# Kernel tuning notes

Measured on AMD Instinct MI355X. Metric: run time of the kernel, lower is better.

## Reference

```python
import jax, jax.numpy as jnp
import numpy as np

LAMBD = 1.0  # margin, matches init kwarg lambd
N, C, D = 16384, 4096, 128


def setup_inputs() -> dict:
    key = jax.random.key(0)
    k1, k2, k3 = jax.random.split(key, 3)
    embeddings = jax.random.normal(k1, (N, D), dtype=jnp.float32)
    targets = jax.random.randint(k2, (N,), 0, C, dtype=jnp.int64)
    centers = jax.random.normal(k3, (C, D), dtype=jnp.float32)
    return {"embeddings": embeddings, "targets": targets, "centers": centers}


def reference(embeddings, targets, centers):
    # Squared euclidean distances from every sample to every center, [n, C],
    # via ||e||^2 + ||c||^2 - 2 e.c (avoids the [n, C, d] broadcast tensor).
    e2 = jnp.sum(embeddings * embeddings, axis=-1, keepdims=True)          # [n, 1]
    c2 = jnp.sum(centers * centers, axis=-1)                               # [C]
    dist = e2 + c2[None, :] - 2.0 * jnp.matmul(embeddings, centers.T)      # [n, C]

    tgt = targets.astype(jnp.int32)
    ap = jnp.take_along_axis(dist, tgt[:, None], axis=1)                   # [n, 1]

    # loss_val[i, c] = lambd + d(e_i, center_{y_i}) - d(e_i, center_c)
    loss_val = LAMBD + ap - dist                                           # [n, C]

    # Triplet (i, y_i, c) is mined iff loss_val > 0 and c != y_i.
    not_label = jnp.arange(dist.shape[1], dtype=jnp.int32)[None, :] != tgt[:, None]
    mask = (loss_val > 0.0) & not_label

    # For mined triplets relu(ap - an + lambd) == loss_val (already > 0).
    total = jnp.sum(jnp.where(mask, loss_val, 0.0))
    cnt = jnp.sum(mask).astype(loss_val.dtype)
    # If no triplet violates the margin, the original returns 0.
    return jnp.where(cnt > 0.0, total / jnp.maximum(cnt, 1.0), 0.0)
```

## Files before the change

kernel.cpp:

```cpp
#include <hip/hip_runtime.h>

#define N_SAMP 16384
#define N_CENT 4096
#define DIM    128
#define LAMBD  1.0f
#define NSLOT  256

typedef _Float16 half8  __attribute__((ext_vector_type(8)));
typedef float    floatx4 __attribute__((ext_vector_type(4)));

struct Slot { float sum; unsigned int cnt; unsigned int pad[30]; };

__device__ __forceinline__ void gload_lds16(const void* g, void* l) {
  __builtin_amdgcn_global_load_lds(
      (__attribute__((address_space(1))) void*)(g),
      (__attribute__((address_space(3))) void*)(l), 16, 0, 0);
}

__global__ __launch_bounds__(256) void prep_kernel(
    const float* __restrict__ E, const float* __restrict__ Cc,
    const int* __restrict__ tgt,
    _Float16* __restrict__ Eh, _Float16* __restrict__ Ch,
    float* __restrict__ c2, float* __restrict__ rowk,
    Slot* __restrict__ slots) {
  const int tid = threadIdx.x;
  const int STAT_BLOCKS = (N_SAMP + N_CENT) / 16;
  if ((int)blockIdx.x < STAT_BLOCKS) {
    if (blockIdx.x == 0) { slots[tid].sum = 0.f; slots[tid].cnt = 0u; }
    const int row   = blockIdx.x * 16 + (tid >> 4);
    const int l16   = tid & 15;
    if (row < N_SAMP) {
      const int yi = tgt[row];
      const float4* e = (const float4*)(E  + (size_t)row * DIM + l16 * 8);
      const float4* c = (const float4*)(Cc + (size_t)yi  * DIM + l16 * 8);
      float4 e0 = e[0], e1 = e[1], c0 = c[0], c1 = c[1];
      float s = c0.x*(c0.x-2.f*e0.x) + c0.y*(c0.y-2.f*e0.y)
              + c0.z*(c0.z-2.f*e0.z) + c0.w*(c0.w-2.f*e0.w)
              + c1.x*(c1.x-2.f*e1.x) + c1.y*(c1.y-2.f*e1.y)
              + c1.z*(c1.z-2.f*e1.z) + c1.w*(c1.w-2.f*e1.w);
      s += __shfl_down(s, 8, 16);
      s += __shfl_down(s, 4, 16);
      s += __shfl_down(s, 2, 16);
      s += __shfl_down(s, 1, 16);
      if (l16 == 0) rowk[row] = LAMBD + s;
    } else {
      const int cI = row - N_SAMP;
      const float4* c = (const float4*)(Cc + (size_t)cI * DIM + l16 * 8);
      float4 c0 = c[0], c1 = c[1];
      float s = c0.x*c0.x + c0.y*c0.y + c0.z*c0.z + c0.w*c0.w
              + c1.x*c1.x + c1.y*c1.y + c1.z*c1.z + c1.w*c1.w;
      s += __shfl_down(s, 8, 16);
      s += __shfl_down(s, 4, 16);
      s += __shfl_down(s, 2, 16);
      s += __shfl_down(s, 1, 16);
      if (l16 == 0) c2[cI] = s;
    }
  } else {
    const int t = ((int)blockIdx.x - STAT_BLOCKS) * 256 + tid;
    const int NE8 = N_SAMP * DIM / 8;
    const float4* src;
    half8* dst;
    int idx;
    if (t < NE8) { src = (const float4*)E;  dst = (half8*)Eh; idx = t; }
    else         { src = (const float4*)Cc; dst = (half8*)Ch; idx = t - NE8; }
    float4 a = src[(size_t)idx * 2], b = src[(size_t)idx * 2 + 1];
    half8 h;
    h[0]=(_Float16)a.x; h[1]=(_Float16)a.y; h[2]=(_Float16)a.z; h[3]=(_Float16)a.w;
    h[4]=(_Float16)b.x; h[5]=(_Float16)b.y; h[6]=(_Float16)b.z; h[7]=(_Float16)b.w;
    dst[idx] = h;
  }
}

__global__ __launch_bounds__(256, 3) void center_gemm_kernel(
    const _Float16* __restrict__ Eh, const _Float16* __restrict__ Ch,
    const float* __restrict__ c2, const float* __restrict__ rowk,
    const int* __restrict__ tgt,
    Slot* __restrict__ slots) {
  __shared__ _Float16 Bs[128 * DIM];
  __shared__ float rowkS[128];
  __shared__ float c2S[128];
  __shared__ int   yS[128];
  __shared__ float swsum[4];
  __shared__ int   swcnt[4];

  const int tid  = threadIdx.x;
  const int w    = tid >> 6;
  const int lane = tid & 63;
  const int q = lane >> 4, r = lane & 15;

  const int bid = blockIdx.x;
  const int xcd = bid & 7;
  const int j   = bid >> 3;
  const int bm  = xcd * 16 + (j & 15);
  const int bn  = j >> 4;

  {
    const char* gB = (const char*)(Ch + (size_t)bn * 128 * DIM);
    char* lB = (char*)Bs;
    const int p  = lane & 15;
    const int r4 = lane >> 4;
    #pragma unroll
    for (int it = 0; it < 8; ++it) {
      const int off = (w * 8 + it) * 1024;
      const int row = (w * 8 + it) * 4 + r4;
      const int gof = row * 256 + (p ^ (row & 15)) * 16;
      gload_lds16(gB + gof, lB + off);
    }
  }

  const int wm = w >> 1, wn = w & 1;
  const int row0 = wm * 64, col0 = wn * 64;
  half8 areg[4][4];
  #pragma unroll
  for (int ks = 0; ks < 4; ++ks)
    #pragma unroll
    for (int mt = 0; mt < 4; ++mt)
      areg[ks][mt] = *(const half8*)&Eh[
          (size_t)(bm * 128 + row0 + mt * 16 + r) * DIM + ks * 32 + q * 8];

  if (tid < 128) {
    rowkS[tid] = rowk[bm * 128 + tid];
    yS[tid]    = tgt[bm * 128 + tid];
    c2S[tid]   = c2[bn * 128 + tid];
  }
  __syncthreads();

  floatx4 acc[4][4];
  #pragma unroll
  for (int a = 0; a < 4; ++a)
    #pragma unroll
    for (int b = 0; b < 4; ++b)
      acc[a][b] = (floatx4){0.f, 0.f, 0.f, 0.f};

  #pragma unroll
  for (int ks = 0; ks < 4; ++ks) {
    const int cidx = ks * 4 + q;
    half8 bf[4];
    #pragma unroll
    for (int nt = 0; nt < 4; ++nt)
      bf[nt] = *(const half8*)&Bs[(col0 + nt * 16 + r) * DIM + ((cidx ^ r) * 8)];
    #pragma unroll
    for (int mt = 0; mt < 4; ++mt)
      #pragma unroll
      for (int nt = 0; nt < 4; ++nt)
        acc[mt][nt] = __builtin_amdgcn_mfma_f32_16x16x32_f16(areg[ks][mt], bf[nt], acc[mt][nt], 0, 0, 0);
  }

  float lsum = 0.f;
  int   lcnt = 0;
  #pragma unroll
  for (int mt = 0; mt < 4; ++mt) {
    float rk[4]; int yv[4];
    #pragma unroll
    for (int rg = 0; rg < 4; ++rg) {
      const int row = row0 + mt * 16 + q * 4 + rg;
      rk[rg] = rowkS[row];
      yv[rg] = yS[row];
    }
    #pragma unroll
    for (int nt = 0; nt < 4; ++nt) {
      const int col  = col0 + nt * 16 + r;
      const float c2v = c2S[col];
      const int gcol = bn * 128 + col;
      #pragma unroll
      for (int rg = 0; rg < 4; ++rg) {
        const float v = rk[rg] + 2.f * acc[mt][nt][rg] - c2v;
        const bool mined = (v > 0.f) & (gcol != yv[rg]);
        lsum += mined ? v : 0.f;
        lcnt += mined ? 1 : 0;
      }
    }
  }

  #pragma unroll
  for (int off = 32; off > 0; off >>= 1) {
    lsum += __shfl_down(lsum, off);
    lcnt += __shfl_down(lcnt, off);
  }
  if (lane == 0) { swsum[w] = lsum; swcnt[w] = lcnt; }
  __syncthreads();
  if (tid == 0) {
    const float s = swsum[0] + swsum[1] + swsum[2] + swsum[3];
    const int   c = swcnt[0] + swcnt[1] + swcnt[2] + swcnt[3];
    Slot* sl = &slots[bid & (NSLOT - 1)];
    atomicAdd(&sl->sum, s);
    atomicAdd(&sl->cnt, (unsigned int)c);
  }
}

__global__ __launch_bounds__(256) void finalize_kernel(
    const Slot* __restrict__ slots, float* __restrict__ out) {
  const int tid = threadIdx.x;
  float s = slots[tid].sum;
  unsigned int c = slots[tid].cnt;
  #pragma unroll
  for (int off = 32; off > 0; off >>= 1) {
    s += __shfl_down(s, off);
    c += __shfl_down(c, off);
  }
  __shared__ float ss[4];
  __shared__ unsigned int sc[4];
  if ((tid & 63) == 0) { ss[tid >> 6] = s; sc[tid >> 6] = c; }
  __syncthreads();
  if (tid == 0) {
    const float S = ss[0] + ss[1] + ss[2] + ss[3];
    const unsigned int C = sc[0] + sc[1] + sc[2] + sc[3];
    out[0] = (C > 0u) ? (S / (float)C) : 0.f;
  }
}

__global__ void zero_kernel(float* ws_sum, unsigned int* ws_cnt) {
  if (threadIdx.x == 0) { *ws_sum = 0.f; *ws_cnt = 0u; }
}

__global__ void finalize_simple(const float* __restrict__ ws_sum,
                                const unsigned int* __restrict__ ws_cnt,
                                float* __restrict__ out) {
  if (threadIdx.x == 0 && blockIdx.x == 0) {
    const unsigned int c = *ws_cnt;
    out[0] = (c > 0u) ? (*ws_sum / (float)c) : 0.f;
  }
}

__global__ __launch_bounds__(256) void fallback_kernel(
    const float* __restrict__ E, const float* __restrict__ Cc,
    const int* __restrict__ tgt,
    float* __restrict__ ws_sum, unsigned int* __restrict__ ws_cnt) {
  __shared__ float eS[DIM];
  __shared__ float apS;
  const int i = blockIdx.x;
  const int tid = threadIdx.x;
  if (tid < DIM) eS[tid] = E[(size_t)i * DIM + tid];
  __syncthreads();
  const int yi = tgt[i];
  float dloc[16];
  #pragma unroll
  for (int j = 0; j < 16; ++j) {
    const int c = tid + 256 * j;
    const float* cp = Cc + (size_t)c * DIM;
    float s = 0.f;
    for (int d = 0; d < DIM; d += 4) {
      float4 cv = *(const float4*)(cp + d);
      s += cv.x * (cv.x - 2.f * eS[d + 0]) + cv.y * (cv.y - 2.f * eS[d + 1])
         + cv.z * (cv.z - 2.f * eS[d + 2]) + cv.w * (cv.w - 2.f * eS[d + 3]);
    }
    dloc[j] = s;
    if (c == yi) apS = s;
  }
  __syncthreads();
  const float apv = apS;
  float lsum = 0.f; int lcnt = 0;
  #pragma unroll
  for (int j = 0; j < 16; ++j) {
    const int c = tid + 256 * j;
    const float v = LAMBD + apv - dloc[j];
    const bool mined = (v > 0.f) & (c != yi);
    lsum += mined ? v : 0.f;
    lcnt += mined ? 1 : 0;
  }
  #pragma unroll
  for (int off = 32; off > 0; off >>= 1) {
    lsum += __shfl_down(lsum, off);
    lcnt += __shfl_down(lcnt, off);
  }
  __shared__ float swsum[4];
  __shared__ int   swcnt[4];
  const int w = tid >> 6, lane = tid & 63;
  if (lane == 0) { swsum[w] = lsum; swcnt[w] = lcnt; }
  __syncthreads();
  if (tid == 0) {
    atomicAdd(ws_sum, swsum[0] + swsum[1] + swsum[2] + swsum[3]);
    atomicAdd(ws_cnt, (unsigned int)(swcnt[0] + swcnt[1] + swcnt[2] + swcnt[3]));
  }
}

extern "C" void kernel_launch(void* const* d_in, const int* in_sizes, int n_in,
                              void* d_out, int out_size, void* d_ws, size_t ws_size,
                              hipStream_t stream) {
  const float* E   = (const float*)d_in[0];
  const int*   tgt = (const int*)d_in[1];
  const float* Cc  = (const float*)d_in[2];
  float* out = (float*)d_out;

  const size_t EH_BYTES = (size_t)N_SAMP * DIM * 2;
  const size_t CH_BYTES = (size_t)N_CENT * DIM * 2;
  const size_t C2_BYTES = (size_t)N_CENT * 4;
  const size_t RK_BYTES = (size_t)N_SAMP * 4;
  const size_t SL_BYTES = (size_t)NSLOT * sizeof(Slot);
  const size_t NEEDED = EH_BYTES + CH_BYTES + C2_BYTES + RK_BYTES + SL_BYTES;

  char* ws = (char*)d_ws;
  if (ws_size >= NEEDED) {
    _Float16* Eh = (_Float16*)ws;
    _Float16* Ch = (_Float16*)(ws + EH_BYTES);
    float* c2    = (float*)(ws + EH_BYTES + CH_BYTES);
    float* rowk  = (float*)(ws + EH_BYTES + CH_BYTES + C2_BYTES);
    Slot* slots  = (Slot*)(ws + EH_BYTES + CH_BYTES + C2_BYTES + RK_BYTES);

    const int STAT_BLOCKS = (N_SAMP + N_CENT) / 16;
    const int CONV_BLOCKS = (N_SAMP * DIM / 8 + N_CENT * DIM / 8) / 256;
    prep_kernel<<<STAT_BLOCKS + CONV_BLOCKS, 256, 0, stream>>>(
        E, Cc, tgt, Eh, Ch, c2, rowk, slots);
    center_gemm_kernel<<<(N_CENT / 128) * (N_SAMP / 128), 256, 0, stream>>>(
        Eh, Ch, c2, rowk, tgt, slots);
    finalize_kernel<<<1, 256, 0, stream>>>(slots, out);
  } else {
    float* ws_sum = (float*)ws;
    unsigned int* ws_cnt = (unsigned int*)(ws_sum + 1);
    zero_kernel<<<1, 64, 0, stream>>>(ws_sum, ws_cnt);
    fallback_kernel<<<N_SAMP, 256, 0, stream>>>(E, Cc, tgt, ws_sum, ws_cnt);
    finalize_simple<<<1, 64, 0, stream>>>(ws_sum, ws_cnt, out);
  }
}
```

Baseline: 104.9 us.

## Process four row chunks per block with double-buffered A registers

Each GEMM block now loads its 128-column center tile into LDS once and reuses it across four 128-row chunks of embeddings (512 rows total), cutting the grid by four. The next chunk's A fragments are prefetched into a second register buffer while the current chunk's MFMAs and epilogue run. This removes repeated center-tile loads and per-block launch and sync overhead. In exchange it raises register pressure (occupancy hint lowered from 3 to 2) and changes the block-to-tile mapping, dropping the earlier XCD-aware swizzle.

```diff
diff --git a/kernel.cpp b/kernel.cpp
--- a/kernel.cpp
+++ b/kernel.cpp
@@ -5,6 +5,7 @@
 #define DIM    128
 #define LAMBD  1.0f
 #define NSLOT  256
+#define NCHUNK 4
 
 typedef _Float16 half8  __attribute__((ext_vector_type(8)));
 typedef float    floatx4 __attribute__((ext_vector_type(4)));
@@ -27,8 +28,8 @@
   const int STAT_BLOCKS = (N_SAMP + N_CENT) / 16;
   if ((int)blockIdx.x < STAT_BLOCKS) {
     if (blockIdx.x == 0) { slots[tid].sum = 0.f; slots[tid].cnt = 0u; }
-    const int row   = blockIdx.x * 16 + (tid >> 4);
-    const int l16   = tid & 15;
+    const int row = blockIdx.x * 16 + (tid >> 4);
+    const int l16 = tid & 15;
     if (row < N_SAMP) {
       const int yi = tgt[row];
       const float4* e = (const float4*)(E  + (size_t)row * DIM + l16 * 8);
@@ -71,15 +72,15 @@
   }
 }
 
-__global__ __launch_bounds__(256, 3) void center_gemm_kernel(
+__global__ __launch_bounds__(256, 2) void center_gemm_kernel(
     const _Float16* __restrict__ Eh, const _Float16* __restrict__ Ch,
     const float* __restrict__ c2, const float* __restrict__ rowk,
     const int* __restrict__ tgt,
     Slot* __restrict__ slots) {
   __shared__ _Float16 Bs[128 * DIM];
-  __shared__ float rowkS[128];
+  __shared__ float rowkS[512];
+  __shared__ int   yS[512];
   __shared__ float c2S[128];
-  __shared__ int   yS[128];
   __shared__ float swsum[4];
   __shared__ int   swcnt[4];
 
@@ -89,10 +90,19 @@
   const int q = lane >> 4, r = lane & 15;
 
   const int bid = blockIdx.x;
-  const int xcd = bid & 7;
-  const int j   = bid >> 3;
-  const int bm  = xcd * 16 + (j & 15);
-  const int bn  = j >> 4;
+  const int bn  = bid & 31;
+  const int bmg = bid >> 5;
+
+  const int wm = w >> 1, wn = w & 1;
+  const int row0 = wm * 64, col0 = wn * 64;
+  const size_t arowbase = (size_t)(bmg * 512 + row0 + r) * DIM + q * 8;
+
+  half8 ar[2][4][4];
+  #pragma unroll
+  for (int ks = 0; ks < 4; ++ks)
+    #pragma unroll
+    for (int mt = 0; mt < 4; ++mt)
+      ar[0][ks][mt] = *(const half8*)&Eh[arowbase + (size_t)(mt * 16) * DIM + ks * 32];
 
   {
     const char* gB = (const char*)(Ch + (size_t)bn * 128 * DIM);
@@ -107,67 +117,71 @@
       gload_lds16(gB + gof, lB + off);
     }
   }
-
-  const int wm = w >> 1, wn = w & 1;
-  const int row0 = wm * 64, col0 = wn * 64;
-  half8 areg[4][4];
-  #pragma unroll
-  for (int ks = 0; ks < 4; ++ks)
-    #pragma unroll
-    for (int mt = 0; mt < 4; ++mt)
-      areg[ks][mt] = *(const half8*)&Eh[
-          (size_t)(bm * 128 + row0 + mt * 16 + r) * DIM + ks * 32 + q * 8];
-
-  if (tid < 128) {
-    rowkS[tid] = rowk[bm * 128 + tid];
-    yS[tid]    = tgt[bm * 128 + tid];
-    c2S[tid]   = c2[bn * 128 + tid];
-  }
-  __syncthreads();
-
-  floatx4 acc[4][4];
-  #pragma unroll
-  for (int a = 0; a < 4; ++a)
-    #pragma unroll
-    for (int b = 0; b < 4; ++b)
-      acc[a][b] = (floatx4){0.f, 0.f, 0.f, 0.f};
-
-  #pragma unroll
-  for (int ks = 0; ks < 4; ++ks) {
-    const int cidx = ks * 4 + q;
-    half8 bf[4];
-    #pragma unroll
-    for (int nt = 0; nt < 4; ++nt)
-      bf[nt] = *(const half8*)&Bs[(col0 + nt * 16 + r) * DIM + ((cidx ^ r) * 8)];
-    #pragma unroll
-    for (int mt = 0; mt < 4; ++mt)
-      #pragma unroll
-      for (int nt = 0; nt < 4; ++nt)
-        acc[mt][nt] = __builtin_amdgcn_mfma_f32_16x16x32_f16(areg[ks][mt], bf[nt], acc[mt][nt], 0, 0, 0);
-  }
+  rowkS[tid]       = rowk[bmg * 512 + tid];
+  rowkS[tid + 256] = rowk[bmg * 512 + 256 + tid];
+  yS[tid]          = tgt[bmg * 512 + tid];
+  yS[tid + 256]    = tgt[bmg * 512 + 256 + tid];
+  if (tid < 128) c2S[tid] = c2[bn * 128 + tid];
+  __syncthreads();
 
   float lsum = 0.f;
   int   lcnt = 0;
-  #pragma unroll
-  for (int mt = 0; mt < 4; ++mt) {
-    float rk[4]; int yv[4];
-    #pragma unroll
-    for (int rg = 0; rg < 4; ++rg) {
-      const int row = row0 + mt * 16 + q * 4 + rg;
-      rk[rg] = rowkS[row];
-      yv[rg] = yS[row];
-    }
-    #pragma unroll
-    for (int nt = 0; nt < 4; ++nt) {
-      const int col  = col0 + nt * 16 + r;
-      const float c2v = c2S[col];
-      const int gcol = bn * 128 + col;
+
+  #pragma unroll
+  for (int c = 0; c < NCHUNK; ++c) {
+    const int cur = c & 1, nxt = cur ^ 1;
+
+    floatx4 acc[4][4];
+    #pragma unroll
+    for (int a = 0; a < 4; ++a)
+      #pragma unroll
+      for (int b = 0; b < 4; ++b)
+        acc[a][b] = (floatx4){0.f, 0.f, 0.f, 0.f};
+    #pragma unroll
+    for (int ks = 0; ks < 4; ++ks) {
+      const int cidx = ks * 4 + q;
+      half8 bf[4];
+      #pragma unroll
+      for (int nt = 0; nt < 4; ++nt)
+        bf[nt] = *(const half8*)&Bs[(col0 + nt * 16 + r) * DIM + ((cidx ^ r) * 8)];
+      #pragma unroll
+      for (int mt = 0; mt < 4; ++mt)
+        #pragma unroll
+        for (int nt = 0; nt < 4; ++nt)
+          acc[mt][nt] = __builtin_amdgcn_mfma_f32_16x16x32_f16(ar[cur][ks][mt], bf[nt], acc[mt][nt], 0, 0, 0);
+    }
+
+    if (c + 1 < NCHUNK) {
+      const size_t base = arowbase + (size_t)((c + 1) * 128) * DIM;
+      #pragma unroll
+      for (int ks = 0; ks < 4; ++ks)
+        #pragma unroll
+        for (int mt = 0; mt < 4; ++mt)
+          ar[nxt][ks][mt] = *(const half8*)&Eh[base + (size_t)(mt * 16) * DIM + ks * 32];
+    }
+
+    const int rbase = c * 128 + row0;
+    #pragma unroll
+    for (int mt = 0; mt < 4; ++mt) {
+      float rk[4]; int yv[4];
       #pragma unroll
       for (int rg = 0; rg < 4; ++rg) {
-        const float v = rk[rg] + 2.f * acc[mt][nt][rg] - c2v;
-        const bool mined = (v > 0.f) & (gcol != yv[rg]);
-        lsum += mined ? v : 0.f;
-        lcnt += mined ? 1 : 0;
+        const int rowi = rbase + mt * 16 + q * 4 + rg;
+        rk[rg] = rowkS[rowi];
+        yv[rg] = yS[rowi];
+      }
+      #pragma unroll
+      for (int nt = 0; nt < 4; ++nt) {
+        const int col  = col0 + nt * 16 + r;
+        const float c2v = c2S[col];
+        const int gcol = bn * 128 + col;
+        #pragma unroll
+        for (int rg = 0; rg < 4; ++rg) {
+          const float v = rk[rg] + 2.f * acc[mt][nt][rg] - c2v;
+          const bool mined = (v > 0.f) & (gcol != yv[rg]);
+          lsum += mined ? v : 0.f;
+          lcnt += mined ? 1 : 0;
+        }
       }
     }
   }
@@ -301,7 +315,7 @@
     const int CONV_BLOCKS = (N_SAMP * DIM / 8 + N_CENT * DIM / 8) / 256;
     prep_kernel<<<STAT_BLOCKS + CONV_BLOCKS, 256, 0, stream>>>(
         E, Cc, tgt, Eh, Ch, c2, rowk, slots);
-    center_gemm_kernel<<<(N_CENT / 128) * (N_SAMP / 128), 256, 0, stream>>>(
+    center_gemm_kernel<<<(N_CENT / 128) * (N_SAMP / 512), 256, 0, stream>>>(
         Eh, Ch, c2, rowk, tgt, slots);
     finalize_kernel<<<1, 256, 0, stream>>>(slots, out);
   } else {
```

After: 105.0 us. Within noise of the previous version (+0.1%).

## Fuse fp16 conversion into GEMM and drop label mask via diagonal correction

Applied to the files above, without the earlier changes.

Removes the separate fp32-to-fp16 conversion pass and its workspace buffers. The GEMM now loads fp32 tiles of both embeddings and centers, converts them in registers and stores them swizzled into LDS. The per-element label check is dropped. Instead, rowk is computed from fp16-rounded values so each sample's own-center term equals exactly lambda, and the finalize step subtracts N*lambda and N from the sum and count. This saves a global read/write pass and per-element compares. It costs LDS usage (occupancy hint drops from 3 to 2), redundant fp32 loads of E across 32 column tiles, and correctness that depends on the own-center term matching the MFMA result bit-exactly.

```diff
diff --git a/kernel.cpp b/kernel.cpp
--- a/kernel.cpp
+++ b/kernel.cpp
@@ -11,75 +11,63 @@
 
 struct Slot { float sum; unsigned int cnt; unsigned int pad[30]; };
 
-__device__ __forceinline__ void gload_lds16(const void* g, void* l) {
-  __builtin_amdgcn_global_load_lds(
-      (__attribute__((address_space(1))) void*)(g),
-      (__attribute__((address_space(3))) void*)(l), 16, 0, 0);
-}
-
 __global__ __launch_bounds__(256) void prep_kernel(
     const float* __restrict__ E, const float* __restrict__ Cc,
     const int* __restrict__ tgt,
-    _Float16* __restrict__ Eh, _Float16* __restrict__ Ch,
     float* __restrict__ c2, float* __restrict__ rowk,
     Slot* __restrict__ slots) {
   const int tid = threadIdx.x;
-  const int STAT_BLOCKS = (N_SAMP + N_CENT) / 16;
-  if ((int)blockIdx.x < STAT_BLOCKS) {
-    if (blockIdx.x == 0) { slots[tid].sum = 0.f; slots[tid].cnt = 0u; }
-    const int row   = blockIdx.x * 16 + (tid >> 4);
-    const int l16   = tid & 15;
-    if (row < N_SAMP) {
-      const int yi = tgt[row];
-      const float4* e = (const float4*)(E  + (size_t)row * DIM + l16 * 8);
-      const float4* c = (const float4*)(Cc + (size_t)yi  * DIM + l16 * 8);
-      float4 e0 = e[0], e1 = e[1], c0 = c[0], c1 = c[1];
-      float s = c0.x*(c0.x-2.f*e0.x) + c0.y*(c0.y-2.f*e0.y)
-              + c0.z*(c0.z-2.f*e0.z) + c0.w*(c0.w-2.f*e0.w)
-              + c1.x*(c1.x-2.f*e1.x) + c1.y*(c1.y-2.f*e1.y)
-              + c1.z*(c1.z-2.f*e1.z) + c1.w*(c1.w-2.f*e1.w);
-      s += __shfl_down(s, 8, 16);
-      s += __shfl_down(s, 4, 16);
-      s += __shfl_down(s, 2, 16);
-      s += __shfl_down(s, 1, 16);
-      if (l16 == 0) rowk[row] = LAMBD + s;
-    } else {
-      const int cI = row - N_SAMP;
-      const float4* c = (const float4*)(Cc + (size_t)cI * DIM + l16 * 8);
-      float4 c0 = c[0], c1 = c[1];
-      float s = c0.x*c0.x + c0.y*c0.y + c0.z*c0.z + c0.w*c0.w
-              + c1.x*c1.x + c1.y*c1.y + c1.z*c1.z + c1.w*c1.w;
-      s += __shfl_down(s, 8, 16);
-      s += __shfl_down(s, 4, 16);
-      s += __shfl_down(s, 2, 16);
-      s += __shfl_down(s, 1, 16);
-      if (l16 == 0) c2[cI] = s;
-    }
+  if (blockIdx.x == 0) { slots[tid].sum = 0.f; slots[tid].cnt = 0u; }
+  const int row = blockIdx.x * 16 + (tid >> 4);
+  const int l16 = tid & 15;
+  if (row < N_SAMP) {
+    const int yi = tgt[row];
+    const float4* ep = (const float4*)(E  + (size_t)row * DIM + l16 * 8);
+    const float4* cp = (const float4*)(Cc + (size_t)yi  * DIM + l16 * 8);
+    float4 e0 = ep[0], e1 = ep[1], c0 = cp[0], c1 = cp[1];
+    float s = 0.f;
+    {
+      float ev[8] = {e0.x,e0.y,e0.z,e0.w,e1.x,e1.y,e1.z,e1.w};
+      float cv[8] = {c0.x,c0.y,c0.z,c0.w,c1.x,c1.y,c1.z,c1.w};
+      #pragma unroll
+      for (int k = 0; k < 8; ++k) {
+        float eh = (float)(_Float16)ev[k];
+        float ch = (float)(_Float16)cv[k];
+        s += ch * (ch - 2.f * eh);
+      }
+    }
+    s += __shfl_down(s, 8, 16);
+    s += __shfl_down(s, 4, 16);
+    s += __shfl_down(s, 2, 16);
+    s += __shfl_down(s, 1, 16);
+    if (l16 == 0) rowk[row] = LAMBD + s;
   } else {
-    const int t = ((int)blockIdx.x - STAT_BLOCKS) * 256 + tid;
-    const int NE8 = N_SAMP * DIM / 8;
-    const float4* src;
-    half8* dst;
-    int idx;
-    if (t < NE8) { src = (const float4*)E;  dst = (half8*)Eh; idx = t; }
-    else         { src = (const float4*)Cc; dst = (half8*)Ch; idx = t - NE8; }
-    float4 a = src[(size_t)idx * 2], b = src[(size_t)idx * 2 + 1];
-    half8 h;
-    h[0]=(_Float16)a.x; h[1]=(_Float16)a.y; h[2]=(_Float16)a.z; h[3]=(_Float16)a.w;
-    h[4]=(_Float16)b.x; h[5]=(_Float16)b.y; h[6]=(_Float16)b.z; h[7]=(_Float16)b.w;
-    dst[idx] = h;
-  }
-}
-
-__global__ __launch_bounds__(256, 3) void center_gemm_kernel(
-    const _Float16* __restrict__ Eh, const _Float16* __restrict__ Ch,
+    const int cI = row - N_SAMP;
+    const float4* cp = (const float4*)(Cc + (size_t)cI * DIM + l16 * 8);
+    float4 c0 = cp[0], c1 = cp[1];
+    float cv[8] = {c0.x,c0.y,c0.z,c0.w,c1.x,c1.y,c1.z,c1.w};
+    float s = 0.f;
+    #pragma unroll
+    for (int k = 0; k < 8; ++k) {
+      float ch = (float)(_Float16)cv[k];
+      s += ch * ch;
+    }
+    s += __shfl_down(s, 8, 16);
+    s += __shfl_down(s, 4, 16);
+    s += __shfl_down(s, 2, 16);
+    s += __shfl_down(s, 1, 16);
+    if (l16 == 0) c2[cI] = s;
+  }
+}
+
+__global__ __launch_bounds__(256, 2) void center_gemm_kernel(
+    const float* __restrict__ E, const float* __restrict__ Cc,
     const float* __restrict__ c2, const float* __restrict__ rowk,
-    const int* __restrict__ tgt,
     Slot* __restrict__ slots) {
+  __shared__ _Float16 As[128 * DIM];
   __shared__ _Float16 Bs[128 * DIM];
   __shared__ float rowkS[128];
   __shared__ float c2S[128];
-  __shared__ int   yS[128];
   __shared__ float swsum[4];
   __shared__ int   swcnt[4];
 
@@ -89,41 +77,39 @@
   const int q = lane >> 4, r = lane & 15;
 
   const int bid = blockIdx.x;
-  const int xcd = bid & 7;
-  const int j   = bid >> 3;
-  const int bm  = xcd * 16 + (j & 15);
-  const int bn  = j >> 4;
+  const int bn  = bid & 31;
+  const int bm  = bid >> 5;
 
   {
-    const char* gB = (const char*)(Ch + (size_t)bn * 128 * DIM);
-    char* lB = (char*)Bs;
-    const int p  = lane & 15;
-    const int r4 = lane >> 4;
-    #pragma unroll
-    for (int it = 0; it < 8; ++it) {
-      const int off = (w * 8 + it) * 1024;
-      const int row = (w * 8 + it) * 4 + r4;
-      const int gof = row * 256 + (p ^ (row & 15)) * 16;
-      gload_lds16(gB + gof, lB + off);
-    }
-  }
+    const int sr = tid >> 1;
+    const int h  = tid & 1;
+    const int sw = (sr & 15);
+    const float4* srcA = (const float4*)(E  + (size_t)(bm * 128 + sr) * DIM + h * 64);
+    const float4* srcB = (const float4*)(Cc + (size_t)(bn * 128 + sr) * DIM + h * 64);
+    _Float16* dstA = As + sr * DIM;
+    _Float16* dstB = Bs + sr * DIM;
+    #pragma unroll
+    for (int k = 0; k < 8; ++k) {
+      float4 a0 = srcA[k * 2], a1 = srcA[k * 2 + 1];
+      half8 ha;
+      ha[0]=(_Float16)a0.x; ha[1]=(_Float16)a0.y; ha[2]=(_Float16)a0.z; ha[3]=(_Float16)a0.w;
+      ha[4]=(_Float16)a1.x; ha[5]=(_Float16)a1.y; ha[6]=(_Float16)a1.z; ha[7]=(_Float16)a1.w;
+      *(half8*)(dstA + (((h * 8 + k) ^ sw) * 8)) = ha;
+      float4 b0 = srcB[k * 2], b1 = srcB[k * 2 + 1];
+      half8 hb;
+      hb[0]=(_Float16)b0.x; hb[1]=(_Float16)b0.y; hb[2]=(_Float16)b0.z; hb[3]=(_Float16)b0.w;
+      hb[4]=(_Float16)b1.x; hb[5]=(_Float16)b1.y; hb[6]=(_Float16)b1.z; hb[7]=(_Float16)b1.w;
+      *(half8*)(dstB + (((h * 8 + k) ^ sw) * 8)) = hb;
+    }
+  }
+  if (tid < 128) {
+    rowkS[tid] = rowk[bm * 128 + tid];
+    c2S[tid]   = c2[bn * 128 + tid];
+  }
+  __syncthreads();
 
   const int wm = w >> 1, wn = w & 1;
   const int row0 = wm * 64, col0 = wn * 64;
-  half8 areg[4][4];
-  #pragma unroll
-  for (int ks = 0; ks < 4; ++ks)
-    #pragma unroll
-    for (int mt = 0; mt < 4; ++mt)
-      areg[ks][mt] = *(const half8*)&Eh[
-          (size_t)(bm * 128 + row0 + mt * 16 + r) * DIM + ks * 32 + q * 8];
-
-  if (tid < 128) {
-    rowkS[tid] = rowk[bm * 128 + tid];
-    yS[tid]    = tgt[bm * 128 + tid];
-    c2S[tid]   = c2[bn * 128 + tid];
-  }
-  __syncthreads();
 
   floatx4 acc[4][4];
   #pragma unroll
@@ -135,7 +121,10 @@
   #pragma unroll
   for (int ks = 0; ks < 4; ++ks) {
     const int cidx = ks * 4 + q;
-    half8 bf[4];
+    half8 af[4], bf[4];
+    #pragma unroll
+    for (int mt = 0; mt < 4; ++mt)
+      af[mt] = *(const half8*)&As[(row0 + mt * 16 + r) * DIM + ((cidx ^ r) * 8)];
     #pragma unroll
     for (int nt = 0; nt < 4; ++nt)
       bf[nt] = *(const half8*)&Bs[(col0 + nt * 16 + r) * DIM + ((cidx ^ r) * 8)];
@@ -143,31 +132,25 @@
     for (int mt = 0; mt < 4; ++mt)
       #pragma unroll
       for (int nt = 0; nt < 4; ++nt)
-        acc[mt][nt] = __builtin_amdgcn_mfma_f32_16x16x32_f16(areg[ks][mt], bf[nt], acc[mt][nt], 0, 0, 0);
+        acc[mt][nt] = __builtin_amdgcn_mfma_f32_16x16x32_f16(af[mt], bf[nt], acc[mt][nt], 0, 0, 0);
   }
 
   float lsum = 0.f;
   int   lcnt = 0;
   #pragma unroll
   for (int mt = 0; mt < 4; ++mt) {
-    float rk[4]; int yv[4];
-    #pragma unroll
-    for (int rg = 0; rg < 4; ++rg) {
-      const int row = row0 + mt * 16 + q * 4 + rg;
-      rk[rg] = rowkS[row];
-      yv[rg] = yS[row];
-    }
+    float rk[4];
+    #pragma unroll
+    for (int rg = 0; rg < 4; ++rg)
+      rk[rg] = rowkS[row0 + mt * 16 + q * 4 + rg];
     #pragma unroll
     for (int nt = 0; nt < 4; ++nt) {
-      const int col  = col0 + nt * 16 + r;
-      const float c2v = c2S[col];
-      const int gcol = bn * 128 + col;
+      const float c2v = c2S[col0 + nt * 16 + r];
       #pragma unroll
       for (int rg = 0; rg < 4; ++rg) {
-        const float v = rk[rg] + 2.f * acc[mt][nt][rg] - c2v;
-        const bool mined = (v > 0.f) & (gcol != yv[rg]);
-        lsum += mined ? v : 0.f;
-        lcnt += mined ? 1 : 0;
+        const float v = fmaf(2.f, acc[mt][nt][rg], rk[rg] - c2v);
+        lsum += fmaxf(v, 0.f);
+        lcnt += (v > 0.f) ? 1 : 0;
       }
     }
   }
@@ -203,9 +186,9 @@
   if ((tid & 63) == 0) { ss[tid >> 6] = s; sc[tid >> 6] = c; }
   __syncthreads();
   if (tid == 0) {
-    const float S = ss[0] + ss[1] + ss[2] + ss[3];
-    const unsigned int C = sc[0] + sc[1] + sc[2] + sc[3];
-    out[0] = (C > 0u) ? (S / (float)C) : 0.f;
+    const float S = ss[0] + ss[1] + ss[2] + ss[3] - (float)N_SAMP * LAMBD;
+    const float C = (float)(ss ? (sc[0] + sc[1] + sc[2] + sc[3]) : 0u) - (float)N_SAMP;
+    out[0] = (C > 0.f) ? (S / C) : 0.f;
   }
 }
 
@@ -282,27 +265,21 @@
   const float* Cc  = (const float*)d_in[2];
   float* out = (float*)d_out;
 
-  const size_t EH_BYTES = (size_t)N_SAMP * DIM * 2;
-  const size_t CH_BYTES = (size_t)N_CENT * DIM * 2;
   const size_t C2_BYTES = (size_t)N_CENT * 4;
   const size_t RK_BYTES = (size_t)N_SAMP * 4;
   const size_t SL_BYTES = (size_t)NSLOT * sizeof(Slot);
-  const size_t NEEDED = EH_BYTES + CH_BYTES + C2_BYTES + RK_BYTES + SL_BYTES;
+  const size_t NEEDED = C2_BYTES + RK_BYTES + SL_BYTES;
 
   char* ws = (char*)d_ws;
   if (ws_size >= NEEDED) {
-    _Float16* Eh = (_Float16*)ws;
-    _Float16* Ch = (_Float16*)(ws + EH_BYTES);
-    float* c2    = (float*)(ws + EH_BYTES + CH_BYTES);
-    float* rowk  = (float*)(ws + EH_BYTES + CH_BYTES + C2_BYTES);
-    Slot* slots  = (Slot*)(ws + EH_BYTES + CH_BYTES + C2_BYTES + RK_BYTES);
-
-    const int STAT_BLOCKS = (N_SAMP + N_CENT) / 16;
-    const int CONV_BLOCKS = (N_SAMP * DIM / 8 + N_CENT * DIM / 8) / 256;
-    prep_kernel<<<STAT_BLOCKS + CONV_BLOCKS, 256, 0, stream>>>(
-        E, Cc, tgt, Eh, Ch, c2, rowk, slots);
+    float* c2   = (float*)ws;
+    float* rowk = (float*)(ws + C2_BYTES);
+    Slot* slots = (Slot*)(ws + C2_BYTES + RK_BYTES);
+
+    prep_kernel<<<(N_SAMP + N_CENT) / 16, 256, 0, stream>>>(
+        E, Cc, tgt, c2, rowk, slots);
     center_gemm_kernel<<<(N_CENT / 128) * (N_SAMP / 128), 256, 0, stream>>>(
-        Eh, Ch, c2, rowk, tgt, slots);
+        E, Cc, c2, rowk, slots);
     finalize_kernel<<<1, 256, 0, stream>>>(slots, out);
   } else {
     float* ws_sum = (float*)ws;
```

Result: slower. 132.6 us (+26.4%).
